# Kernel tuning notes

Hardware: AMD Instinct MI355X
Metric: run time of the kernel (lower is better)

Reference implementation:

```python
import jax, jax.numpy as jnp
import numpy as np

EPS = 1e-12

def _smooth_clamp(x, x_lb, x_rb, slope_l, slope_r):
    # Smoothly saturating clamp onto [x_lb, x_rb] with linear tails of the given slopes.
    t = (x - x_lb) / (x_rb - x_lb)
    core = x_lb + (x_rb - x_lb) * jax.nn.sigmoid(4.0 * t - 2.0)
    return core + slope_l * jnp.minimum(x - x_lb, 0.0) + slope_r * jnp.maximum(x - x_rb, 0.0)

def _rot_mat_to_quat_wxyz(R):
    # R: [..., 3, 3] -> q: [..., 4] (W,X,Y,Z), robust 4-case formula, vectorized.
    m00, m01, m02 = R[..., 0, 0], R[..., 0, 1], R[..., 0, 2]
    m10, m11, m12 = R[..., 1, 0], R[..., 1, 1], R[..., 1, 2]
    m20, m21, m22 = R[..., 2, 0], R[..., 2, 1], R[..., 2, 2]
    tr = m00 + m11 + m22
    t0 = jnp.maximum(1.0 + tr, 1e-8)
    t1 = jnp.maximum(1.0 + m00 - m11 - m22, 1e-8)
    t2 = jnp.maximum(1.0 - m00 + m11 - m22, 1e-8)
    t3 = jnp.maximum(1.0 - m00 - m11 + m22, 1e-8)
    s0 = 0.5 / jnp.sqrt(t0)
    s1 = 0.5 / jnp.sqrt(t1)
    s2 = 0.5 / jnp.sqrt(t2)
    s3 = 0.5 / jnp.sqrt(t3)
    q0 = jnp.stack([t0, m21 - m12, m02 - m20, m10 - m01], -1) * s0[..., None]
    q1 = jnp.stack([m21 - m12, t1, m01 + m10, m02 + m20], -1) * s1[..., None]
    q2 = jnp.stack([m02 - m20, m01 + m10, t2, m12 + m21], -1) * s2[..., None]
    q3 = jnp.stack([m10 - m01, m02 + m20, m12 + m21, t3], -1) * s3[..., None]
    idx = jnp.argmax(jnp.stack([tr, m00, m11, m22], -1), -1)[..., None]
    q = jnp.where(idx == 0, q0, jnp.where(idx == 1, q1, jnp.where(idx == 2, q2, q3)))
    return q

def _quat_mul_wxyz(p, q):
    pw, px, py, pz = p[..., 0], p[..., 1], p[..., 2], p[..., 3]
    qw, qx, qy, qz = q[..., 0], q[..., 1], q[..., 2], q[..., 3]
    return jnp.stack([
        pw * qw - px * qx - py * qy - pz * qz,
        pw * qx + px * qw + py * qz - pz * qy,
        pw * qy - px * qz + py * qw + pz * qx,
        pw * qz + px * qy - py * qx + pz * qw,
    ], -1)

def setup_inputs() -> dict:
    key = jax.random.key(0)
    ks = jax.random.split(key, 9)
    F = 2_000_000
    return {
        'vert_pos_a': jax.random.normal(ks[0], (F, 3), jnp.float32),
        'vert_pos_b': jax.random.normal(ks[1], (F, 3), jnp.float32),
        'vert_pos_c': jax.random.normal(ks[2], (F, 3), jnp.float32),
        'gp_rot_z': jax.random.normal(ks[3], (F,), jnp.float32),
        'gp_scale_x': jax.random.normal(ks[4], (F,), jnp.float32) - 3.0,
        'gp_scale_y': jax.random.normal(ks[5], (F,), jnp.float32) - 3.0,
        'gp_scale_z': jax.random.normal(ks[6], (F,), jnp.float32) - 3.0,
        'gp_color': jax.random.uniform(ks[7], (F, 3), jnp.float32),
        'gp_log_opacity': jax.random.normal(ks[8], (F,), jnp.float32),
    }

def reference(vert_pos_a, vert_pos_b, vert_pos_c, gp_rot_z,
              gp_scale_x, gp_scale_y, gp_scale_z, gp_color, gp_log_opacity):
    # --- per-face coordinate frame (get_face_coord) ---
    e1 = vert_pos_b - vert_pos_a                     # [F,3]
    e2 = vert_pos_c - vert_pos_a                     # [F,3]
    n = jnp.cross(e1, e2)                            # [F,3]
    n_norm = jnp.linalg.norm(n, axis=-1)             # [F]
    area = 0.5 * n_norm                              # [F]
    ax = e1 / (jnp.linalg.norm(e1, axis=-1, keepdims=True) + EPS)
    az = n / (n_norm[..., None] + EPS)
    ay = jnp.cross(az, ax)
    R = jnp.stack([ax, ay, az], -1)                  # [F,3,3], columns = axes
    t = (vert_pos_a + vert_pos_b + vert_pos_c) / 3.0 # centroid, [F,3]

    # --- quaternions ---
    face_q = _rot_mat_to_quat_wxyz(R)                # [F,4] WXYZ
    half = gp_rot_z * 0.5
    zeros = jnp.zeros_like(half)
    local_q = jnp.stack([jnp.cos(half), zeros, zeros, jnp.sin(half)], -1)
    world_q = _quat_mul_wxyz(face_q, local_q)        # [F,4]

    # --- scales ---
    sf = jnp.sqrt(area)                              # [F]
    sx = sf * _smooth_clamp(jnp.exp(gp_scale_x), 0.1, 3.0, 0.0, 0.005)
    sy = sf * _smooth_clamp(jnp.exp(gp_scale_y), 0.1, 3.0, 0.0, 0.005)
    sz = _smooth_clamp(sf * jnp.exp(gp_scale_z), 0.001, 0.01, 0.0, 0.005)
    scale = jnp.stack([sx, sy, sz], -1)              # [F,3]

    opacity = jnp.exp(gp_log_opacity)                # [F]

    # concat outputs: mean(3) | quat(4) | scale(3) | color(3) | opacity(1) -> [F,14]
    return jnp.concatenate([t, world_q, scale, gp_color, opacity[..., None]], -1)
```

## Files before the change

### kernel.cpp

```cpp
#include <hip/hip_runtime.h>
#include <math.h>

#define EPS 1e-12f

typedef float f32x4 __attribute__((ext_vector_type(4)));

__device__ __forceinline__ float smooth_clamp(float x, float lb, float rb, float sr) {
    float t = (x - lb) / (rb - lb);
    float sig = 1.0f / (1.0f + __expf(-(4.0f * t - 2.0f)));
    float core = lb + (rb - lb) * sig;
    return core + sr * fmaxf(x - rb, 0.0f);
}

__device__ __forceinline__ void compute_face(
    int i,
    const float* __restrict__ pa, const float* __restrict__ pb, const float* __restrict__ pc,
    const float* __restrict__ rotz,
    const float* __restrict__ gsx, const float* __restrict__ gsy, const float* __restrict__ gsz,
    const float* __restrict__ color, const float* __restrict__ lop,
    float* __restrict__ sr)
{
    float pax = pa[3*i+0], pay = pa[3*i+1], paz = pa[3*i+2];
    float pbx = pb[3*i+0], pby = pb[3*i+1], pbz = pb[3*i+2];
    float pcx = pc[3*i+0], pcy = pc[3*i+1], pcz = pc[3*i+2];

    float e1x = pbx - pax, e1y = pby - pay, e1z = pbz - paz;
    float e2x = pcx - pax, e2y = pcy - pay, e2z = pcz - paz;
    float nx = e1y*e2z - e1z*e2y;
    float ny = e1z*e2x - e1x*e2z;
    float nz = e1x*e2y - e1y*e2x;
    float nn = sqrtf(nx*nx + ny*ny + nz*nz);
    float area = 0.5f * nn;

    float e1n = sqrtf(e1x*e1x + e1y*e1y + e1z*e1z);
    float inv_e1 = 1.0f / (e1n + EPS);
    float axx = e1x*inv_e1, axy = e1y*inv_e1, axz = e1z*inv_e1;
    float inv_n = 1.0f / (nn + EPS);
    float azx = nx*inv_n, azy = ny*inv_n, azz = nz*inv_n;
    float ayx = azy*axz - azz*axy;
    float ayy = azz*axx - azx*axz;
    float ayz = azx*axy - azy*axx;

    float m00 = axx, m01 = ayx, m02 = azx;
    float m10 = axy, m11 = ayy, m12 = azy;
    float m20 = axz, m21 = ayz, m22 = azz;

    float tr = m00 + m11 + m22;
    float t0 = fmaxf(1.0f + tr,              1e-8f);
    float t1 = fmaxf(1.0f + m00 - m11 - m22, 1e-8f);
    float t2 = fmaxf(1.0f - m00 + m11 - m22, 1e-8f);
    float t3 = fmaxf(1.0f - m00 - m11 + m22, 1e-8f);

    int idx = 0; float best = tr;
    if (m00 > best) { best = m00; idx = 1; }
    if (m11 > best) { best = m11; idx = 2; }
    if (m22 > best) { idx = 3; }

    float qw, qx, qy, qz;
    if (idx == 0) {
        float sN = 0.5f * rsqrtf(t0);
        qw = t0*sN; qx = (m21-m12)*sN; qy = (m02-m20)*sN; qz = (m10-m01)*sN;
    } else if (idx == 1) {
        float sN = 0.5f * rsqrtf(t1);
        qw = (m21-m12)*sN; qx = t1*sN; qy = (m01+m10)*sN; qz = (m02+m20)*sN;
    } else if (idx == 2) {
        float sN = 0.5f * rsqrtf(t2);
        qw = (m02-m20)*sN; qx = (m01+m10)*sN; qy = t2*sN; qz = (m12+m21)*sN;
    } else {
        float sN = 0.5f * rsqrtf(t3);
        qw = (m10-m01)*sN; qx = (m02+m20)*sN; qy = (m12+m21)*sN; qz = t3*sN;
    }

    float half = 0.5f * rotz[i];
    float sh, ch;
    __sincosf(half, &sh, &ch);
    float wqw = qw*ch - qz*sh;
    float wqx = qx*ch + qy*sh;
    float wqy = qy*ch - qx*sh;
    float wqz = qw*sh + qz*ch;

    float sf = sqrtf(area);
    float sx = sf * smooth_clamp(__expf(gsx[i]), 0.1f,   3.0f, 0.005f);
    float sy = sf * smooth_clamp(__expf(gsy[i]), 0.1f,   3.0f, 0.005f);
    float sz =      smooth_clamp(sf * __expf(gsz[i]), 0.001f, 0.01f, 0.005f);

    float opacity = __expf(lop[i]);

    float cr = color[3*i+0], cg = color[3*i+1], cb = color[3*i+2];

    float tx = (pax + pbx + pcx) * (1.0f/3.0f);
    float ty = (pay + pby + pcy) * (1.0f/3.0f);
    float tz = (paz + pbz + pcz) * (1.0f/3.0f);

    sr[0]  = tx;  sr[1]  = ty;  sr[2]  = tz;
    sr[3]  = wqw; sr[4]  = wqx; sr[5]  = wqy; sr[6]  = wqz;
    sr[7]  = sx;  sr[8]  = sy;  sr[9]  = sz;
    sr[10] = cr;  sr[11] = cg;  sr[12] = cb;  sr[13] = opacity;
}

__global__ void __launch_bounds__(256) face_kernel(
    const float* __restrict__ pa, const float* __restrict__ pb, const float* __restrict__ pc,
    const float* __restrict__ rotz,
    const float* __restrict__ gsx, const float* __restrict__ gsy, const float* __restrict__ gsz,
    const float* __restrict__ color, const float* __restrict__ lop,
    float* __restrict__ out, int F)
{
    __shared__ float s[512 * 14];

    const int tid = threadIdx.x;
    const int blockBase = blockIdx.x * 512;
    const int i0 = blockBase + tid;
    const int i1 = blockBase + 256 + tid;
    const int count = min(512, F - blockBase);

    if (i0 < F) compute_face(i0, pa, pb, pc, rotz, gsx, gsy, gsz, color, lop, &s[tid * 14]);
    if (i1 < F) compute_face(i1, pa, pb, pc, rotz, gsx, gsy, gsz, color, lop, &s[(256 + tid) * 14]);

    __syncthreads();

    const int nfloat = count * 14;
    float* obase = out + (long)blockBase * 14;
    const int nf4 = nfloat >> 2;
    #pragma unroll 2
    for (int j = tid; j < nf4; j += 256) {
        f32x4 v = *reinterpret_cast<const f32x4*>(&s[4*j]);
        __builtin_nontemporal_store(v, reinterpret_cast<f32x4*>(obase) + j);
    }
    const int rem = nfloat & 3;
    if (tid < rem) {
        obase[nf4*4 + tid] = s[nf4*4 + tid];
    }
}

extern "C" void kernel_launch(void* const* d_in, const int* in_sizes, int n_in,
                              void* d_out, int out_size, void* d_ws, size_t ws_size,
                              hipStream_t stream) {
    const float* pa   = (const float*)d_in[0];
    const float* pb   = (const float*)d_in[1];
    const float* pc   = (const float*)d_in[2];
    const float* rotz = (const float*)d_in[3];
    const float* gsx  = (const float*)d_in[4];
    const float* gsy  = (const float*)d_in[5];
    const float* gsz  = (const float*)d_in[6];
    const float* col  = (const float*)d_in[7];
    const float* lop  = (const float*)d_in[8];
    float* out = (float*)d_out;

    int F = in_sizes[3];
    int block = 256;
    int grid = (F + 511) / 512;
    face_kernel<<<grid, block, 0, stream>>>(pa, pb, pc, rotz, gsx, gsy, gsz, col, lop, out, F);
}
```

Baseline: 40.91 us.

## Replace block barrier with per-wave LDS staging and one face per thread

Each thread now computes one face instead of two, and each 64-lane wave writes out only the 64 faces it staged itself. The block-wide __syncthreads is replaced by an inline s_waitcnt lgkmcnt(0), so waves do not wait on each other. The grid doubles and LDS per block halves, which may raise occupancy. The approach depends on wavefront-synchronous execution and on the compiler not reordering LDS accesses around the inline asm. It also loses the per-thread memory-level parallelism that came from handling two faces per thread.

```diff
diff --git a/kernel.cpp b/kernel.cpp
--- a/kernel.cpp
+++ b/kernel.cpp
@@ -105,30 +105,35 @@
     const float* __restrict__ color, const float* __restrict__ lop,
     float* __restrict__ out, int F)
 {
-    __shared__ float s[512 * 14];
+    __shared__ float s[256 * 14];
 
-    const int tid = threadIdx.x;
-    const int blockBase = blockIdx.x * 512;
-    const int i0 = blockBase + tid;
-    const int i1 = blockBase + 256 + tid;
-    const int count = min(512, F - blockBase);
+    const int tid  = threadIdx.x;
+    const int wave = tid >> 6;
+    const int lane = tid & 63;
+    const int blockBase = blockIdx.x * 256;
+    const int i = blockBase + tid;
 
-    if (i0 < F) compute_face(i0, pa, pb, pc, rotz, gsx, gsy, gsz, color, lop, &s[tid * 14]);
-    if (i1 < F) compute_face(i1, pa, pb, pc, rotz, gsx, gsy, gsz, color, lop, &s[(256 + tid) * 14]);
+    if (i < F) {
+        compute_face(i, pa, pb, pc, rotz, gsx, gsy, gsz, color, lop, &s[tid * 14]);
+    }
 
-    __syncthreads();
+    __asm__ volatile("s_waitcnt lgkmcnt(0)" ::: "memory");
 
-    const int nfloat = count * 14;
-    float* obase = out + (long)blockBase * 14;
-    const int nf4 = nfloat >> 2;
-    #pragma unroll 2
-    for (int j = tid; j < nf4; j += 256) {
-        f32x4 v = *reinterpret_cast<const f32x4*>(&s[4*j]);
-        __builtin_nontemporal_store(v, reinterpret_cast<f32x4*>(obase) + j);
-    }
-    const int rem = nfloat & 3;
-    if (tid < rem) {
-        obase[nf4*4 + tid] = s[nf4*4 + tid];
+    const int waveBase = blockBase + wave * 64;
+    const int nface = min(64, F - waveBase);
+    if (nface > 0) {
+        const int nfloat = nface * 14;
+        const int nf4 = nfloat >> 2;
+        float* obase = out + (long)waveBase * 14;
+        const float* sbase = &s[wave * 896];
+        for (int j = lane; j < nf4; j += 64) {
+            f32x4 v = *reinterpret_cast<const f32x4*>(&sbase[4*j]);
+            __builtin_nontemporal_store(v, reinterpret_cast<f32x4*>(obase) + j);
+        }
+        const int rem = nfloat & 3;
+        if (lane < rem) {
+            obase[nf4*4 + lane] = sbase[nf4*4 + lane];
+        }
     }
 }
 
@@ -148,6 +153,6 @@
 
     int F = in_sizes[3];
     int block = 256;
-    int grid = (F + 511) / 512;
+    int grid = (F + 255) / 256;
     face_kernel<<<grid, block, 0, stream>>>(pa, pb, pc, rotz, gsx, gsy, gsz, col, lop, out, F);
 }
```

Measured after the change: 41.81 us. +2.2%, slower.
